# Performance work log

Hardware: AMD Instinct MI355X
Metric: run time of the kernel (lower is better)

The kernel has to match this reference:

```python
import jax, jax.numpy as jnp
import numpy as np

IN_FEATURES = 4096
OUT_FEATURES = 11008
BATCH = 64


def setup_inputs() -> dict:
    key = jax.random.key(0)
    k_x, k_w, k_s, k_b = jax.random.split(key, 4)
    x = jax.random.normal(k_x, (BATCH, IN_FEATURES), dtype=jnp.float32)
    # int8-range quantized weights stored as int8 (symmetric, [-128, 127])
    weight_q = jax.random.randint(k_w, (OUT_FEATURES, IN_FEATURES), -128, 128, dtype=jnp.int8)
    # per-output-row scales, strictly positive (absmax/127 style)
    scale = jax.random.uniform(k_s, (OUT_FEATURES, 1), dtype=jnp.float32, minval=1e-4, maxval=2e-2)
    bias = jax.random.normal(k_b, (OUT_FEATURES,), dtype=jnp.float32)
    return {"x": x, "weight_q": weight_q, "scale": scale, "bias": bias}


def reference(x, weight_q, scale, bias):
    # on-the-fly dequantization: w_deq[o, i] = weight_q[o, i] * scale[o]
    w_deq = weight_q.astype(x.dtype) * scale.astype(x.dtype)  # [O, I]
    # F.linear: y = x @ w_deq.T + bias
    return jnp.einsum('bi,oi->bo', x, w_deq) + bias
```

## Files before the change

kernel.cpp:

```cpp
#include <hip/hip_runtime.h>

#define IN_F 4096
#define OUT_F 11008
#define BATCH 64
#define NT (OUT_F / 16)
#define NSTEP (IN_F / 64)
#define KS 8
#define SPW (NSTEP / KS)

typedef int v4i __attribute__((ext_vector_type(4)));
typedef float v4f __attribute__((ext_vector_type(4)));
typedef signed char i8;

#define WS_XQ 0u
#define WS_XS (256u * 1024u)
#define WS_WB (257u * 1024u)
#define WS_PART (WS_WB + (size_t)OUT_F * IN_F)

__device__ __forceinline__ int pack4(int a0, int a1, int a2, int a3) {
    return (a0 & 0xff) | ((a1 & 0xff) << 8) | ((a2 & 0xff) << 16) |
           ((unsigned)a3 << 24);
}

__global__ __launch_bounds__(256)
void quant_x_kernel(const float* __restrict__ x, i8* __restrict__ xq,
                    float* __restrict__ xscale)
{
    const int b = blockIdx.x;
    const int t = threadIdx.x;
    const float* xr = x + (size_t)b * IN_F;
    const int i0 = t * 16;

    float vals[16];
    float m = 0.0f;
#pragma unroll
    for (int j = 0; j < 16; ++j) {
        vals[j] = xr[i0 + j];
        m = fmaxf(m, fabsf(vals[j]));
    }

    __shared__ float red[256];
    red[t] = m;
    __syncthreads();
    for (int s = 128; s > 0; s >>= 1) {
        if (t < s) red[t] = fmaxf(red[t], red[t + s]);
        __syncthreads();
    }
    const float amax = red[0];
    const float inv = (amax > 0.0f) ? (127.0f / amax) : 0.0f;
    if (t == 0) xscale[b] = (amax > 0.0f) ? (amax / 127.0f) : 1.0f;

    const int kc   = i0 >> 6;
    const int quad = (i0 >> 4) & 3;
    const int mt   = b >> 4;
    const int lane = (b & 15) | (quad << 4);

    i8 q[16];
#pragma unroll
    for (int j = 0; j < 16; ++j) {
        float r = rintf(vals[j] * inv);
        r = fminf(127.0f, fmaxf(-127.0f, r));
        q[j] = (i8)(int)r;
    }
    *(v4i*)(xq + ((size_t)(kc * 256 + mt * 64 + lane) * 16)) = *(const v4i*)q;
}

__global__ __launch_bounds__(256)
void pack_w_kernel(const int* __restrict__ wq, i8* __restrict__ wb)
{
    const int nt = blockIdx.y;
    const int sg = blockIdx.x;
    const int t  = threadIdx.x;
    const int row = t >> 4;
    const int c   = t & 15;

    __shared__ int lds[4 * 272];

    const int* base = wq + (size_t)(nt * 16 + row) * IN_F + sg * 256 + c * 4;
#pragma unroll
    for (int r = 0; r < 4; ++r) {
        v4i w = *(const v4i*)(base + r * 64);
        lds[r * 272 + row * 17 + c] = pack4(w[0], w[1], w[2], w[3]);
    }
    __syncthreads();

    const int sl = t >> 6;
    const int L  = t & 63;
    const int n  = t & 15;
    const int q  = (t >> 4) & 3;
    v4i o;
#pragma unroll
    for (int d = 0; d < 4; ++d)
        o[d] = lds[sl * 272 + n * 17 + q * 4 + d];
    *(v4i*)(wb + ((size_t)(nt * 64 + sg * 4 + sl) * 64 + L) * 16) = o;
}

__global__ __launch_bounds__(256)
void gemm_kernel(const i8* __restrict__ wb, const i8* __restrict__ xq,
                 const float* __restrict__ xscale,
                 const float* __restrict__ wscale,
                 float* __restrict__ part)
{
    const int lane = threadIdx.x & 63;
    const int wave = threadIdx.x >> 6;
    const int nt   = blockIdx.x * 4 + wave;
    const int ks   = blockIdx.y;

    const v4i* pB = (const v4i*)wb + ((size_t)nt * 64 + ks * SPW) * 64 + lane;
    const v4i* pA = (const v4i*)xq + (size_t)(ks * SPW) * 256 + lane;

    v4i acc[4];
#pragma unroll
    for (int mt = 0; mt < 4; ++mt) acc[mt] = (v4i){0, 0, 0, 0};

    v4i bC, bN, aC[4], aN[4];
    bC = pB[0];
#pragma unroll
    for (int mt = 0; mt < 4; ++mt) aC[mt] = pA[mt * 64];

#pragma unroll
    for (int ss = 0; ss < SPW; ++ss) {
        if (ss + 1 < SPW) {
            bN = pB[(size_t)(ss + 1) * 64];
#pragma unroll
            for (int mt = 0; mt < 4; ++mt) aN[mt] = pA[(size_t)(ss + 1) * 256 + mt * 64];
        }
#pragma unroll
        for (int mt = 0; mt < 4; ++mt)
            acc[mt] = __builtin_amdgcn_mfma_i32_16x16x64_i8(aC[mt], bC, acc[mt], 0, 0, 0);
        if (ss + 1 < SPW) {
            bC = bN;
#pragma unroll
            for (int mt = 0; mt < 4; ++mt) aC[mt] = aN[mt];
        }
    }

    const int n = lane & 15;
    const int o = nt * 16 + n;
    const float wsc = wscale[o];
    const int rbase = (lane >> 4) * 4;
    float* pp = part + (size_t)ks * BATCH * OUT_F + o;
#pragma unroll
    for (int mt = 0; mt < 4; ++mt) {
#pragma unroll
        for (int r = 0; r < 4; ++r) {
            const int brow = mt * 16 + rbase + r;
            pp[(size_t)brow * OUT_F] = (float)acc[mt][r] * xscale[brow] * wsc;
        }
    }
}

__global__ __launch_bounds__(256)
void reduce_kernel(const float* __restrict__ part, const float* __restrict__ bias,
                   float* __restrict__ out)
{
    const int i = (blockIdx.x * 256 + threadIdx.x) * 4;
    const int o = i % OUT_F;
    v4f s = *(const v4f*)(bias + o);
#pragma unroll
    for (int ks = 0; ks < KS; ++ks)
        s += *(const v4f*)(part + (size_t)ks * BATCH * OUT_F + i);
    *(v4f*)(out + i) = s;
}

extern "C" void kernel_launch(void* const* d_in, const int* in_sizes, int n_in,
                              void* d_out, int out_size, void* d_ws, size_t ws_size,
                              hipStream_t stream)
{
    const float* x      = (const float*)d_in[0];
    const int*   wq     = (const int*)d_in[1];
    const float* wscale = (const float*)d_in[2];
    const float* bias   = (const float*)d_in[3];
    float* out = (float*)d_out;

    i8*    xq     = (i8*)d_ws + WS_XQ;
    float* xscale = (float*)((char*)d_ws + WS_XS);
    i8*    wb     = (i8*)d_ws + WS_WB;
    float* partials = (float*)((char*)d_ws + WS_PART);

    quant_x_kernel<<<BATCH, 256, 0, stream>>>(x, xq, xscale);
    pack_w_kernel<<<dim3(16, NT), 256, 0, stream>>>(wq, wb);
    gemm_kernel<<<dim3(NT / 4, KS), 256, 0, stream>>>(wb, xq, xscale, wscale, partials);
    reduce_kernel<<<(BATCH * OUT_F) / 1024, 256, 0, stream>>>(partials, bias, out);
}
```

Measured before the change: 275.9 us.

## Fuse weight packing into GEMM and replace split-K partials with in-block LDS reduction

Drops the separate weight-packing kernel and the split-K reduce kernel. The GEMM now reads the int32-stored weights directly, packs them to int8 MFMA fragments in per-wave LDS, and splits K across the four waves of a block. The per-wave accumulators are summed in LDS, and scale and bias are applied before writing the output. This removes writing and re-reading the packed weight buffer and the partial-sum buffer, plus two launches. In exchange, each step of the GEMM inner loop now does an LDS transpose and pack, and each block covers only 16 output columns.

```diff
diff --git a/kernel.cpp b/kernel.cpp
--- a/kernel.cpp
+++ b/kernel.cpp
@@ -4,18 +4,10 @@
 #define OUT_F 11008
 #define BATCH 64
 #define NT (OUT_F / 16)
-#define NSTEP (IN_F / 64)
-#define KS 8
-#define SPW (NSTEP / KS)
+#define SPW 16
 
 typedef int v4i __attribute__((ext_vector_type(4)));
-typedef float v4f __attribute__((ext_vector_type(4)));
 typedef signed char i8;
-
-#define WS_XQ 0u
-#define WS_XS (256u * 1024u)
-#define WS_WB (257u * 1024u)
-#define WS_PART (WS_WB + (size_t)OUT_F * IN_F)
 
 __device__ __forceinline__ int pack4(int a0, int a1, int a2, int a3) {
     return (a0 & 0xff) | ((a1 & 0xff) << 8) | ((a2 & 0xff) << 16) |
@@ -66,101 +58,95 @@
 }
 
 __global__ __launch_bounds__(256)
-void pack_w_kernel(const int* __restrict__ wq, i8* __restrict__ wb)
-{
-    const int nt = blockIdx.y;
-    const int sg = blockIdx.x;
-    const int t  = threadIdx.x;
-    const int row = t >> 4;
-    const int c   = t & 15;
-
-    __shared__ int lds[4 * 272];
-
-    const int* base = wq + (size_t)(nt * 16 + row) * IN_F + sg * 256 + c * 4;
-#pragma unroll
-    for (int r = 0; r < 4; ++r) {
-        v4i w = *(const v4i*)(base + r * 64);
-        lds[r * 272 + row * 17 + c] = pack4(w[0], w[1], w[2], w[3]);
-    }
-    __syncthreads();
-
-    const int sl = t >> 6;
-    const int L  = t & 63;
-    const int n  = t & 15;
-    const int q  = (t >> 4) & 3;
-    v4i o;
-#pragma unroll
-    for (int d = 0; d < 4; ++d)
-        o[d] = lds[sl * 272 + n * 17 + q * 4 + d];
-    *(v4i*)(wb + ((size_t)(nt * 64 + sg * 4 + sl) * 64 + L) * 16) = o;
-}
-
-__global__ __launch_bounds__(256)
-void gemm_kernel(const i8* __restrict__ wb, const i8* __restrict__ xq,
+void gemm_kernel(const int* __restrict__ wq, const i8* __restrict__ xq,
                  const float* __restrict__ xscale,
                  const float* __restrict__ wscale,
-                 float* __restrict__ part)
+                 const float* __restrict__ bias,
+                 float* __restrict__ out)
 {
+    __shared__ int lds[4 * 1088];
     const int lane = threadIdx.x & 63;
     const int wave = threadIdx.x >> 6;
-    const int nt   = blockIdx.x * 4 + wave;
-    const int ks   = blockIdx.y;
+    const int nt   = blockIdx.x;
+    int* wlds = lds + wave * 1088;
 
-    const v4i* pB = (const v4i*)wb + ((size_t)nt * 64 + ks * SPW) * 64 + lane;
-    const v4i* pA = (const v4i*)xq + (size_t)(ks * SPW) * 256 + lane;
+    const int n    = lane & 15;
+    const int q    = lane >> 4;
+    const int grow = lane >> 4;
+    const int gcol = (lane & 15) * 4;
+
+    const int s0 = wave * SPW;
+    const int* wbase = wq + (size_t)(nt * 16) * IN_F + s0 * 64 + gcol;
+    const v4i* pA = (const v4i*)xq + (size_t)s0 * 256 + lane;
 
     v4i acc[4];
 #pragma unroll
     for (int mt = 0; mt < 4; ++mt) acc[mt] = (v4i){0, 0, 0, 0};
 
-    v4i bC, bN, aC[4], aN[4];
-    bC = pB[0];
+    v4i wC[4], wN[4], aC[4], aN[4];
+#pragma unroll
+    for (int p = 0; p < 4; ++p)
+        wC[p] = *(const v4i*)(wbase + (size_t)(4 * p + grow) * IN_F);
 #pragma unroll
     for (int mt = 0; mt < 4; ++mt) aC[mt] = pA[mt * 64];
 
-#pragma unroll
     for (int ss = 0; ss < SPW; ++ss) {
         if (ss + 1 < SPW) {
-            bN = pB[(size_t)(ss + 1) * 64];
+            const int* nb = wbase + (ss + 1) * 64;
 #pragma unroll
-            for (int mt = 0; mt < 4; ++mt) aN[mt] = pA[(size_t)(ss + 1) * 256 + mt * 64];
+            for (int p = 0; p < 4; ++p)
+                wN[p] = *(const v4i*)(nb + (size_t)(4 * p + grow) * IN_F);
+#pragma unroll
+            for (int mt = 0; mt < 4; ++mt)
+                aN[mt] = pA[(ss + 1) * 256 + mt * 64];
         }
 #pragma unroll
+        for (int p = 0; p < 4; ++p)
+            *(v4i*)(wlds + (4 * p + grow) * 68 + gcol) = wC[p];
+        asm volatile("s_waitcnt lgkmcnt(0)" ::: "memory");
+        v4i rd[4];
+#pragma unroll
+        for (int d = 0; d < 4; ++d)
+            rd[d] = *(const v4i*)(wlds + n * 68 + q * 16 + 4 * d);
+        asm volatile("s_waitcnt lgkmcnt(0)" ::: "memory");
+
+        v4i bfrag;
+#pragma unroll
+        for (int d = 0; d < 4; ++d)
+            bfrag[d] = pack4(rd[d][0], rd[d][1], rd[d][2], rd[d][3]);
+
+#pragma unroll
         for (int mt = 0; mt < 4; ++mt)
-            acc[mt] = __builtin_amdgcn_mfma_i32_16x16x64_i8(aC[mt], bC, acc[mt], 0, 0, 0);
+            acc[mt] = __builtin_amdgcn_mfma_i32_16x16x64_i8(aC[mt], bfrag, acc[mt], 0, 0, 0);
+
         if (ss + 1 < SPW) {
-            bC = bN;
+#pragma unroll
+            for (int p = 0; p < 4; ++p) wC[p] = wN[p];
 #pragma unroll
             for (int mt = 0; mt < 4; ++mt) aC[mt] = aN[mt];
         }
     }
 
-    const int n = lane & 15;
+#pragma unroll
+    for (int mt = 0; mt < 4; ++mt)
+#pragma unroll
+        for (int r = 0; r < 4; ++r)
+            wlds[lane * 17 + mt * 4 + r] = acc[mt][r];
+    __syncthreads();
+
+    const int mt2 = wave;
     const int o = nt * 16 + n;
     const float wsc = wscale[o];
-    const int rbase = (lane >> 4) * 4;
-    float* pp = part + (size_t)ks * BATCH * OUT_F + o;
+    const float bo  = bias[o];
 #pragma unroll
-    for (int mt = 0; mt < 4; ++mt) {
+    for (int r = 0; r < 4; ++r) {
+        int s = 0;
 #pragma unroll
-        for (int r = 0; r < 4; ++r) {
-            const int brow = mt * 16 + rbase + r;
-            pp[(size_t)brow * OUT_F] = (float)acc[mt][r] * xscale[brow] * wsc;
-        }
+        for (int w = 0; w < 4; ++w)
+            s += lds[w * 1088 + lane * 17 + mt2 * 4 + r];
+        const int b = mt2 * 16 + q * 4 + r;
+        out[(size_t)b * OUT_F + o] = (float)s * xscale[b] * wsc + bo;
     }
-}
-
-__global__ __launch_bounds__(256)
-void reduce_kernel(const float* __restrict__ part, const float* __restrict__ bias,
-                   float* __restrict__ out)
-{
-    const int i = (blockIdx.x * 256 + threadIdx.x) * 4;
-    const int o = i % OUT_F;
-    v4f s = *(const v4f*)(bias + o);
-#pragma unroll
-    for (int ks = 0; ks < KS; ++ks)
-        s += *(const v4f*)(part + (size_t)ks * BATCH * OUT_F + i);
-    *(v4f*)(out + i) = s;
 }
 
 extern "C" void kernel_launch(void* const* d_in, const int* in_sizes, int n_in,
@@ -173,13 +159,9 @@
     const float* bias   = (const float*)d_in[3];
     float* out = (float*)d_out;
 
-    i8*    xq     = (i8*)d_ws + WS_XQ;
-    float* xscale = (float*)((char*)d_ws + WS_XS);
-    i8*    wb     = (i8*)d_ws + WS_WB;
-    float* partials = (float*)((char*)d_ws + WS_PART);
+    i8*    xq     = (i8*)d_ws;
+    float* xscale = (float*)((char*)d_ws + 256u * 1024u);
 
     quant_x_kernel<<<BATCH, 256, 0, stream>>>(x, xq, xscale);
-    pack_w_kernel<<<dim3(16, NT), 256, 0, stream>>>(wq, wb);
-    gemm_kernel<<<dim3(NT / 4, KS), 256, 0, stream>>>(wb, xq, xscale, wscale, partials);
-    reduce_kernel<<<(BATCH * OUT_F) / 1024, 256, 0, stream>>>(partials, bias, out);
+    gemm_kernel<<<NT, 256, 0, stream>>>(wq, xq, xscale, wscale, bias, out);
 }
```

Result: faster. 267.7 us (-3.0%).
